# Kernel tuning notes

Hardware: AMD Instinct MI355X
Metric: run time of the kernel (lower is better)

Reference implementation:

```python
import jax, jax.numpy as jnp
import numpy as np

N_PROTS = 2048
MOLS_PER_PROT = 8
N_MOLS = N_PROTS * MOLS_PER_PROT
DIM = 768
MARGIN = 0.5


def setup_inputs() -> dict:
    key = jax.random.key(0)
    k1, k2, k3 = jax.random.split(key, 3)
    prot_emb = jax.random.normal(k1, (N_PROTS, DIM), dtype=jnp.float32)
    mol_emb = jax.random.normal(k2, (N_MOLS, DIM), dtype=jnp.float32)
    # L2-normalize like typical CLIP-style retrieval embeddings
    prot_emb = prot_emb / jnp.linalg.norm(prot_emb, axis=1, keepdims=True)
    mol_emb = mol_emb / jnp.linalg.norm(mol_emb, axis=1, keepdims=True)
    # block-structured labels: protein i paired with mols [8i, 8i+8)
    rows = jnp.repeat(jnp.arange(N_PROTS), MOLS_PER_PROT)
    cols = jnp.arange(N_MOLS)
    labels = jnp.zeros((N_PROTS, N_MOLS), dtype=jnp.float32).at[rows, cols].set(1.0)
    # pIC50 values in [2, 10]
    pic50_matrix = 2.0 + 8.0 * jax.random.uniform(k3, (N_PROTS, N_MOLS), dtype=jnp.float32)
    logit_scale = jnp.float32(1.0 / 0.07)
    return {"prot_emb": prot_emb, "mol_emb": mol_emb, "labels": labels,
            "pic50_matrix": pic50_matrix, "logit_scale": logit_scale}


def reference(prot_emb, mol_emb, labels, pic50_matrix, logit_scale):
    n_prots = prot_emb.shape[0]
    n_mols = mol_emb.shape[0]
    sim = jnp.matmul(prot_emb, mol_emb.T) * logit_scale  # [n_prots, n_mols]

    # affinity-weighted InfoNCE (prot -> mol)
    pic50_norm = jnp.clip((pic50_matrix - 2.0) / 8.0, 0.0, 1.0)
    pos_w = labels * pic50_norm
    pos_w = pos_w / (pos_w.sum(axis=1, keepdims=True) + 1e-8)
    loss_p2m = -jnp.sum(pos_w * jax.nn.log_softmax(sim, axis=1)) / n_prots

    # mol -> prot NLL
    mol_labels = jnp.argmax(labels, axis=0)  # [n_mols]
    lsm_m2p = jax.nn.log_softmax(sim.T, axis=1)  # [n_mols, n_prots]
    loss_m2p = -jnp.mean(lsm_m2p[jnp.arange(n_mols), mol_labels])

    # pairwise margin-ranking among positives (exactly MOLS_PER_PROT positives per protein)
    P = MOLS_PER_PROT
    _, pos_idx = jax.lax.top_k(labels, P)  # [n_prots, P] indices of positives
    pos_pic = jnp.take_along_axis(pic50_matrix, pos_idx, axis=1)  # [n_prots, P]
    pos_sc = jnp.take_along_axis(sim, pos_idx, axis=1)            # [n_prots, P]
    dp = pos_pic[:, :, None] - pos_pic[:, None, :]  # [n_prots, P, P]
    ds = pos_sc[:, :, None] - pos_sc[:, None, :]
    pair = jnp.where(dp > 0, jax.nn.relu(MARGIN - ds),
                     jnp.where(dp < 0, jax.nn.relu(MARGIN + ds), 0.0))
    upper = jnp.triu(jnp.ones((P, P), dtype=bool), k=1)  # unordered pairs j<k
    n_pairs = n_prots * (P * (P - 1) // 2)
    ranking_loss = jnp.sum(jnp.where(upper[None], pair, 0.0)) / n_pairs

    # negative push-down
    neg_loss = jnp.mean(jax.nn.relu(sim * (1.0 - labels)))

    total = loss_p2m + loss_m2p + 0.5 * ranking_loss + 0.1 * neg_loss
    return (total, loss_p2m, loss_m2p, ranking_loss, neg_loss)
```

## Files before the change

kernel.cpp:

```cpp
#include <hip/hip_runtime.h>
#include <hip/hip_bf16.h>
#include <math.h>

#define N_PROTS 2048
#define N_MOLS  16384
#define DIM     768
#define SHIFT   16.0f
#define MARGIN  0.5f

typedef __attribute__((ext_vector_type(8))) short short8;
typedef __attribute__((ext_vector_type(4))) float f32x4;
typedef __attribute__((ext_vector_type(4))) unsigned short us4;
typedef __attribute__((ext_vector_type(8))) unsigned short us8;

__device__ __forceinline__ unsigned short bf16rnd(float x) {
    unsigned int u = __float_as_uint(x);
    u += 0x7fffu + ((u >> 16) & 1u);
    return (unsigned short)(u >> 16);
}

__device__ __forceinline__ void gload16(const void* g, void* l) {
    __builtin_amdgcn_global_load_lds(
        (const __attribute__((address_space(1))) unsigned int*)g,
        (__attribute__((address_space(3))) unsigned int*)l, 16, 0, 0);
}

#define ACC_FLOATS 34824
#define PROT_BF_OFF_B 139296ull
#define PROT_BF_BYTES (2048ull*768*2)
#define MOL_BF_OFF_B  (PROT_BF_OFF_B + PROT_BF_BYTES)
#define MOL_BF_BYTES  (16384ull*768*2)
#define WS_NEED       (MOL_BF_OFF_B + MOL_BF_BYTES)

__global__ __launch_bounds__(256)
void convert_bf16(const float* __restrict__ prot, const float* __restrict__ mol,
                  unsigned short* __restrict__ protBf, unsigned short* __restrict__ molBf)
{
    const size_t PROT_G = (size_t)N_PROTS * DIM / 8;
    size_t t = (size_t)blockIdx.x * 256 + threadIdx.x;
    const float* src;
    unsigned short* dst;
    if (t < PROT_G) { src = prot + t * 8; dst = protBf + t * 8; }
    else            { size_t u = t - PROT_G; src = mol + u * 8; dst = molBf + u * 8; }
    float4 v0 = ((const float4*)src)[0];
    float4 v1 = ((const float4*)src)[1];
    us8 o;
    o[0] = bf16rnd(v0.x); o[1] = bf16rnd(v0.y); o[2] = bf16rnd(v0.z); o[3] = bf16rnd(v0.w);
    o[4] = bf16rnd(v1.x); o[5] = bf16rnd(v1.y); o[6] = bf16rnd(v1.z); o[7] = bf16rnd(v1.w);
    *(us8*)dst = o;
}

__device__ __forceinline__ void epilogue(
    f32x4 acc[4][4], float scale, int rowBase, int colBase,
    int wave, int lane, int wr, int wc, int l15, int q,
    float* __restrict__ row_se, float* __restrict__ col_se,
    float* __restrict__ pos_sim, float* __restrict__ scalars, float* redBuf)
{
    float rsum[4][4];
    float csum[4] = {0.f, 0.f, 0.f, 0.f};
    float rl = 0.f;
#pragma unroll
    for (int mi = 0; mi < 4; ++mi)
#pragma unroll
        for (int r = 0; r < 4; ++r) rsum[mi][r] = 0.f;

#pragma unroll
    for (int mi = 0; mi < 4; ++mi) {
#pragma unroll
        for (int ni = 0; ni < 4; ++ni) {
#pragma unroll
            for (int r = 0; r < 4; ++r) {
                float sim = acc[mi][ni][r] * scale;
                float e = __expf(sim - SHIFT);
                rsum[mi][r] += e;
                csum[ni] += e;
                rl += fmaxf(sim, 0.f);
                int rg = rowBase + wr + mi * 16 + q * 4 + r;
                int cg = colBase + wc + ni * 16 + l15;
                if ((cg >> 3) == rg) pos_sim[cg] = sim;
            }
        }
    }

#pragma unroll
    for (int mi = 0; mi < 4; ++mi) {
#pragma unroll
        for (int r = 0; r < 4; ++r) {
            float v = rsum[mi][r];
            v += __shfl_xor(v, 1); v += __shfl_xor(v, 2);
            v += __shfl_xor(v, 4); v += __shfl_xor(v, 8);
            if (l15 == 0)
                atomicAdd(&row_se[rowBase + wr + mi * 16 + q * 4 + r], v);
        }
    }
#pragma unroll
    for (int ni = 0; ni < 4; ++ni) {
        float v = csum[ni];
        v += __shfl_xor(v, 16); v += __shfl_xor(v, 32);
        if (q == 0)
            atomicAdd(&col_se[colBase + wc + ni * 16 + l15], v);
    }
#pragma unroll
    for (int m = 1; m < 64; m <<= 1) rl += __shfl_xor(rl, m);
    if (lane == 0) redBuf[wave] = rl;
    __syncthreads();
    if (wave == 0 && lane == 0)
        atomicAdd(&scalars[0], redBuf[0] + redBuf[1] + redBuf[2] + redBuf[3]);
}

__global__ __launch_bounds__(256, 2)
void sim_pass_bf16(const unsigned short* __restrict__ protBf,
                   const unsigned short* __restrict__ molBf,
                   const float* __restrict__ scale_p,
                   float* __restrict__ row_se, float* __restrict__ col_se,
                   float* __restrict__ pos_sim, float* __restrict__ scalars)
{
    __shared__ unsigned short As[128][32];
    __shared__ unsigned short Bs[128][32];
    __shared__ float redBuf[4];

    const int tid = threadIdx.x;
    const int rowBase = blockIdx.y * 128;
    const int colBase = blockIdx.x * 128;
    const int wave = tid >> 6;
    const int lane = tid & 63;
    const int wr = (wave >> 1) * 64;
    const int wc = (wave & 1) * 64;
    const int l15 = lane & 15;
    const int q   = lane >> 4;

    f32x4 acc[4][4];
#pragma unroll
    for (int i = 0; i < 4; ++i)
#pragma unroll
        for (int j = 0; j < 4; ++j) acc[i][j] = (f32x4){0.f, 0.f, 0.f, 0.f};

    const int subRow = tid >> 2;
    const int subCol = (tid & 3) << 3;
    const unsigned short* aP0 = protBf + (size_t)(rowBase + subRow) * DIM + subCol;
    const unsigned short* aP1 = aP0 + (size_t)64 * DIM;
    const unsigned short* bP0 = molBf + (size_t)(colBase + subRow) * DIM + subCol;
    const unsigned short* bP1 = bP0 + (size_t)64 * DIM;
    unsigned short* ldsA = &As[0][0] + (wave << 9);
    unsigned short* ldsB = &Bs[0][0] + (wave << 9);

#pragma unroll 1
    for (int s = 0; s < DIM / 32; ++s) {
        gload16(aP0, ldsA);
        gload16(aP1, ldsA + 2048);
        gload16(bP0, ldsB);
        gload16(bP1, ldsB + 2048);
        aP0 += 32; aP1 += 32; bP0 += 32; bP1 += 32;
        __syncthreads();

        short8 aF[4], bF[4];
#pragma unroll
        for (int mi = 0; mi < 4; ++mi) aF[mi] = *(const short8*)&As[wr + mi * 16 + l15][q * 8];
#pragma unroll
        for (int ni = 0; ni < 4; ++ni) bF[ni] = *(const short8*)&Bs[wc + ni * 16 + l15][q * 8];
#pragma unroll
        for (int mi = 0; mi < 4; ++mi)
#pragma unroll
            for (int ni = 0; ni < 4; ++ni)
                acc[mi][ni] = __builtin_amdgcn_mfma_f32_16x16x32_bf16(aF[mi], bF[ni], acc[mi][ni], 0, 0, 0);
        __syncthreads();
    }

    epilogue(acc, scale_p[0], rowBase, colBase, wave, lane, wr, wc, l15, q,
             row_se, col_se, pos_sim, scalars, redBuf);
}

__global__ __launch_bounds__(256, 2)
void sim_pass(const float* __restrict__ prot, const float* __restrict__ mol,
              const float* __restrict__ scale_p,
              float* __restrict__ row_se, float* __restrict__ col_se,
              float* __restrict__ pos_sim, float* __restrict__ scalars)
{
    __shared__ unsigned short As[128][32];
    __shared__ unsigned short Bs[128][32];
    __shared__ float redBuf[4];

    const int tid = threadIdx.x;
    const int rowBase = blockIdx.y * 128;
    const int colBase = blockIdx.x * 128;
    const int wave = tid >> 6;
    const int lane = tid & 63;
    const int wr = (wave >> 1) * 64;
    const int wc = (wave & 1) * 64;
    const int l15 = lane & 15;
    const int q   = lane >> 4;

    f32x4 acc[4][4];
#pragma unroll
    for (int i = 0; i < 4; ++i)
#pragma unroll
        for (int j = 0; j < 4; ++j) acc[i][j] = (f32x4){0.f, 0.f, 0.f, 0.f};

    const float* aBase = prot + (size_t)rowBase * DIM;
    const float* bBase = mol  + (size_t)colBase * DIM;
    float4 aReg[4], bReg[4];
#pragma unroll
    for (int i = 0; i < 4; ++i) {
        int f = tid + 256 * i;
        int row = f >> 3, c4 = f & 7;
        aReg[i] = *(const float4*)(aBase + (size_t)row * DIM + (c4 << 2));
        bReg[i] = *(const float4*)(bBase + (size_t)row * DIM + (c4 << 2));
    }
#pragma unroll 1
    for (int s = 0; s < DIM / 32; ++s) {
#pragma unroll
        for (int i = 0; i < 4; ++i) {
            int f = tid + 256 * i;
            int row = f >> 3, c4 = f & 7;
            us4 av, bv;
            av.x = bf16rnd(aReg[i].x); av.y = bf16rnd(aReg[i].y);
            av.z = bf16rnd(aReg[i].z); av.w = bf16rnd(aReg[i].w);
            bv.x = bf16rnd(bReg[i].x); bv.y = bf16rnd(bReg[i].y);
            bv.z = bf16rnd(bReg[i].z); bv.w = bf16rnd(bReg[i].w);
            *(us4*)&As[row][c4 << 2] = av;
            *(us4*)&Bs[row][c4 << 2] = bv;
        }
        __syncthreads();
        if (s + 1 < DIM / 32) {
            int k0 = (s + 1) * 32;
#pragma unroll
            for (int i = 0; i < 4; ++i) {
                int f = tid + 256 * i;
                int row = f >> 3, c4 = f & 7;
                aReg[i] = *(const float4*)(aBase + (size_t)row * DIM + k0 + (c4 << 2));
                bReg[i] = *(const float4*)(bBase + (size_t)row * DIM + k0 + (c4 << 2));
            }
        }
        short8 aF[4], bF[4];
#pragma unroll
        for (int mi = 0; mi < 4; ++mi) aF[mi] = *(const short8*)&As[wr + mi * 16 + l15][q * 8];
#pragma unroll
        for (int ni = 0; ni < 4; ++ni) bF[ni] = *(const short8*)&Bs[wc + ni * 16 + l15][q * 8];
#pragma unroll
        for (int mi = 0; mi < 4; ++mi)
#pragma unroll
            for (int ni = 0; ni < 4; ++ni)
                acc[mi][ni] = __builtin_amdgcn_mfma_f32_16x16x32_bf16(aF[mi], bF[ni], acc[mi][ni], 0, 0, 0);
        __syncthreads();
    }

    epilogue(acc, scale_p[0], rowBase, colBase, wave, lane, wr, wc, l15, q,
             row_se, col_se, pos_sim, scalars, redBuf);
}

__global__ __launch_bounds__(256)
void finalize1(const float* __restrict__ row_se, const float* __restrict__ col_se,
               const float* __restrict__ pos_sim, const float* __restrict__ pic50,
               float* __restrict__ scalars)
{
    int j = blockIdx.x * 256 + threadIdx.x;
    float m2p = SHIFT + __logf(col_se[j]) - pos_sim[j];

    float p2m = 0.f, rank = 0.f, prelu = 0.f;
    if ((j & 7) == 0) {
        int i = j >> 3;
        float s[8], pc[8], pr[8];
#pragma unroll
        for (int p = 0; p < 8; ++p) {
            s[p]  = pos_sim[j + p];
            pr[p] = pic50[(size_t)i * N_MOLS + j + p];
            float x = (pr[p] - 2.0f) * 0.125f;
            pc[p] = fminf(fmaxf(x, 0.f), 1.f);
            prelu += fmaxf(s[p], 0.f);
        }
        float wsum = 1e-8f;
#pragma unroll
        for (int p = 0; p < 8; ++p) wsum += pc[p];
        float lse = SHIFT + __logf(row_se[i]);
        float accp = 0.f;
#pragma unroll
        for (int p = 0; p < 8; ++p) accp += pc[p] * (lse - s[p]);
        p2m = accp / wsum;
#pragma unroll
        for (int a = 0; a < 8; ++a)
#pragma unroll
            for (int b = a + 1; b < 8; ++b) {
                float dp = pr[a] - pr[b];
                float ds = s[a] - s[b];
                float v = (dp > 0.f) ? fmaxf(MARGIN - ds, 0.f)
                        : ((dp < 0.f) ? fmaxf(MARGIN + ds, 0.f) : 0.f);
                rank += v;
            }
    }

#pragma unroll
    for (int m = 1; m < 64; m <<= 1) {
        m2p   += __shfl_xor(m2p, m);
        p2m   += __shfl_xor(p2m, m);
        rank  += __shfl_xor(rank, m);
        prelu += __shfl_xor(prelu, m);
    }
    __shared__ float rbuf[4][4];
    int wave = threadIdx.x >> 6, lane = threadIdx.x & 63;
    if (lane == 0) { rbuf[wave][0] = m2p; rbuf[wave][1] = p2m; rbuf[wave][2] = rank; rbuf[wave][3] = prelu; }
    __syncthreads();
    if (threadIdx.x == 0) {
        float a = 0, b = 0, c = 0, d = 0;
        for (int w = 0; w < 4; ++w) { a += rbuf[w][0]; b += rbuf[w][1]; c += rbuf[w][2]; d += rbuf[w][3]; }
        atomicAdd(&scalars[2], a);
        atomicAdd(&scalars[1], b);
        atomicAdd(&scalars[3], c);
        atomicAdd(&scalars[4], d);
    }
}

__global__ void finalize2(const float* __restrict__ scalars, float* __restrict__ out)
{
    float relu_neg = scalars[0] - scalars[4];
    float p2m  = scalars[1] / (float)N_PROTS;
    float m2p  = scalars[2] / (float)N_MOLS;
    float rank = scalars[3] / ((float)N_PROTS * 28.0f);
    float neg  = relu_neg / ((float)N_PROTS * (float)N_MOLS);
    out[0] = p2m + m2p + 0.5f * rank + 0.1f * neg;
    out[1] = p2m;
    out[2] = m2p;
    out[3] = rank;
    out[4] = neg;
}

extern "C" void kernel_launch(void* const* d_in, const int* in_sizes, int n_in,
                              void* d_out, int out_size, void* d_ws, size_t ws_size,
                              hipStream_t stream) {
    const float* prot   = (const float*)d_in[0];
    const float* mol    = (const float*)d_in[1];
    const float* pic50  = (const float*)d_in[3];
    const float* lscale = (const float*)d_in[4];

    float* ws      = (float*)d_ws;
    float* row_se  = ws;
    float* col_se  = ws + 2048;
    float* pos_sim = ws + 2048 + 16384;
    float* scalars = ws + 2048 + 16384 + 16384;

    hipMemsetAsync(d_ws, 0, (size_t)ACC_FLOATS * sizeof(float), stream);

    dim3 grid(N_MOLS / 128, N_PROTS / 128);
    if (ws_size >= WS_NEED) {
        unsigned short* protBf = (unsigned short*)((char*)d_ws + PROT_BF_OFF_B);
        unsigned short* molBf  = (unsigned short*)((char*)d_ws + MOL_BF_OFF_B);
        size_t groups = ((size_t)N_PROTS + N_MOLS) * DIM / 8;
        convert_bf16<<<(unsigned)(groups / 256), 256, 0, stream>>>(prot, mol, protBf, molBf);
        sim_pass_bf16<<<grid, 256, 0, stream>>>(protBf, molBf, lscale, row_se, col_se, pos_sim, scalars);
    } else {
        sim_pass<<<grid, 256, 0, stream>>>(prot, mol, lscale, row_se, col_se, pos_sim, scalars);
    }
    finalize1<<<N_MOLS / 256, 256, 0, stream>>>(row_se, col_se, pos_sim, pic50, scalars);
    finalize2<<<1, 1, 0, stream>>>(scalars, (float*)d_out);
}
```

Measured before the change: 395.3 us.

## Double-buffer LDS tiles with XOR swizzle in bf16 sim pass

```diff
diff --git a/kernel.cpp b/kernel.cpp
--- a/kernel.cpp
+++ b/kernel.cpp
@@ -108,15 +108,15 @@
         atomicAdd(&scalars[0], redBuf[0] + redBuf[1] + redBuf[2] + redBuf[3]);
 }
 
-__global__ __launch_bounds__(256, 2)
+__global__ __launch_bounds__(256, 4)
 void sim_pass_bf16(const unsigned short* __restrict__ protBf,
                    const unsigned short* __restrict__ molBf,
                    const float* __restrict__ scale_p,
                    float* __restrict__ row_se, float* __restrict__ col_se,
                    float* __restrict__ pos_sim, float* __restrict__ scalars)
 {
-    __shared__ unsigned short As[128][32];
-    __shared__ unsigned short Bs[128][32];
+    __shared__ unsigned short As[2][128][32];
+    __shared__ unsigned short Bs[2][128][32];
     __shared__ float redBuf[4];
 
     const int tid = threadIdx.x;
@@ -135,35 +135,50 @@
 #pragma unroll
         for (int j = 0; j < 4; ++j) acc[i][j] = (f32x4){0.f, 0.f, 0.f, 0.f};
 
-    const int subRow = tid >> 2;
-    const int subCol = (tid & 3) << 3;
-    const unsigned short* aP0 = protBf + (size_t)(rowBase + subRow) * DIM + subCol;
+    const int r0   = tid >> 2;
+    const int csrc = ((tid & 3) ^ ((r0 >> 1) & 3)) << 3;
+    const unsigned short* aP0 = protBf + (size_t)(rowBase + r0) * DIM + csrc;
     const unsigned short* aP1 = aP0 + (size_t)64 * DIM;
-    const unsigned short* bP0 = molBf + (size_t)(colBase + subRow) * DIM + subCol;
+    const unsigned short* bP0 = molBf + (size_t)(colBase + r0) * DIM + csrc;
     const unsigned short* bP1 = bP0 + (size_t)64 * DIM;
-    unsigned short* ldsA = &As[0][0] + (wave << 9);
-    unsigned short* ldsB = &Bs[0][0] + (wave << 9);
+    unsigned short* ldsA0 = &As[0][0][0] + (wave << 9);
+    unsigned short* ldsB0 = &Bs[0][0][0] + (wave << 9);
+
+    gload16(aP0, ldsA0);
+    gload16(aP1, ldsA0 + 2048);
+    gload16(bP0, ldsB0);
+    gload16(bP1, ldsB0 + 2048);
 
 #pragma unroll 1
     for (int s = 0; s < DIM / 32; ++s) {
-        gload16(aP0, ldsA);
-        gload16(aP1, ldsA + 2048);
-        gload16(bP0, ldsB);
-        gload16(bP1, ldsB + 2048);
-        aP0 += 32; aP1 += 32; bP0 += 32; bP1 += 32;
+        const int cur = s & 1;
         __syncthreads();
 
+        if (s + 1 < DIM / 32) {
+            const int ko = (s + 1) * 32;
+            const int nb = (cur ^ 1) * 4096;
+            gload16(aP0 + ko, ldsA0 + nb);
+            gload16(aP1 + ko, ldsA0 + nb + 2048);
+            gload16(bP0 + ko, ldsB0 + nb);
+            gload16(bP1 + ko, ldsB0 + nb + 2048);
+        }
+
         short8 aF[4], bF[4];
 #pragma unroll
-        for (int mi = 0; mi < 4; ++mi) aF[mi] = *(const short8*)&As[wr + mi * 16 + l15][q * 8];
-#pragma unroll
-        for (int ni = 0; ni < 4; ++ni) bF[ni] = *(const short8*)&Bs[wc + ni * 16 + l15][q * 8];
+        for (int mi = 0; mi < 4; ++mi) {
+            const int R = wr + mi * 16 + l15;
+            aF[mi] = *(const short8*)&As[cur][R][(q ^ ((R >> 1) & 3)) << 3];
+        }
+#pragma unroll
+        for (int ni = 0; ni < 4; ++ni) {
+            const int R = wc + ni * 16 + l15;
+            bF[ni] = *(const short8*)&Bs[cur][R][(q ^ ((R >> 1) & 3)) << 3];
+        }
 #pragma unroll
         for (int mi = 0; mi < 4; ++mi)
 #pragma unroll
             for (int ni = 0; ni < 4; ++ni)
                 acc[mi][ni] = __builtin_amdgcn_mfma_f32_16x16x32_bf16(aF[mi], bF[ni], acc[mi][ni], 0, 0, 0);
-        __syncthreads();
     }
 
     epilogue(acc, scale_p[0], rowBase, colBase, wave, lane, wr, wc, l15, q,
```

Result: no change. 400.6 us (+1.3%).
